# Kernel tuning notes

Hardware: AMD Instinct MI355X
Metric: run time of the kernel (lower is better)

Reference implementation:

```python
import jax, jax.numpy as jnp
import numpy as np

N_NODES = 50000
N_EDGES = 800000
D = 64
N_LAYERS = 3  # layer_dims = [64, 64, 64, 64]


def setup_inputs() -> dict:
    key = jax.random.key(0)
    ks = jax.random.split(key, 5)
    x = jax.random.normal(ks[0], (N_NODES, D), dtype=jnp.float32)
    edge_index = jax.random.randint(ks[1], (2, N_EDGES), 0, N_NODES, dtype=jnp.int64)
    scale = 1.0 / np.sqrt(D)
    # Per-layer restriction (message) maps, self-loop maps, and biases.
    W_msg = jax.random.normal(ks[2], (N_LAYERS, D, D), dtype=jnp.float32) * scale
    W_self = jax.random.normal(ks[3], (N_LAYERS, D, D), dtype=jnp.float32) * scale
    b = jax.random.normal(ks[4], (N_LAYERS, D), dtype=jnp.float32) * 0.01
    return {"x": x, "edge_index": edge_index, "W_msg": W_msg, "W_self": W_self, "b": b}


def reference(x, edge_index, W_msg, W_self, b):
    """Stacked sheaf conv layers: per-edge gather -> linear restriction ->
    scatter-sum aggregation to destination nodes + self-loop linear + bias,
    with ReLU between layers (none after the final layer)."""
    n = x.shape[0]
    src, dst = edge_index[0], edge_index[1]
    n_layers = W_msg.shape[0]
    for i in range(n_layers):
        msg = x[src] @ W_msg[i]                                   # [E, d] gather + restriction
        agg = jax.ops.segment_sum(msg, dst, num_segments=n)       # [N, d] scatter-add
        x = x @ W_self[i] + agg + b[i]                            # self-loop + aggregate + bias
        if i < n_layers - 1:
            x = jax.nn.relu(x)
    return x
```

## Files before the change

kernel.cpp:

```cpp
#include <hip/hip_runtime.h>

#define D 64

__device__ __forceinline__ unsigned short f2bf(float f) {
    unsigned u = __float_as_uint(f);
    unsigned r = (u + 0x7FFFu + ((u >> 16) & 1u)) >> 16;
    return (unsigned short)r;
}
__device__ __forceinline__ float bf2f(unsigned short h) {
    return __uint_as_float((unsigned)h << 16);
}

typedef __attribute__((ext_vector_type(8))) short bf16x8;
typedef __attribute__((ext_vector_type(4))) float f32x4;

__global__ void prep_kernel(const float* __restrict__ x, unsigned short* __restrict__ xb,
                            int total, int* __restrict__ deg, int N,
                            const float* __restrict__ Wself,
                            const float* __restrict__ Wmsg,
                            unsigned short* __restrict__ Bt, int n_layers) {
    int i = blockIdx.x * blockDim.x + threadIdx.x;
    if (i < N) deg[i] = 0;
    int wtotal = n_layers * D * 2 * D;
    if (i < wtotal) {
        int k = i & 127;
        int n = (i >> 7) & 63;
        int l = i >> 13;
        float w = (k < D) ? Wself[(size_t)l * D * D + k * D + n]
                          : Wmsg [(size_t)l * D * D + (k - D) * D + n];
        unsigned short hi = f2bf(w);
        unsigned short lo = f2bf(w - bf2f(hi));
        size_t base = (size_t)l * 2 * D * 2 * D;
        Bt[base + (size_t)n * 128 + k] = hi;
        Bt[base + 8192 + (size_t)n * 128 + k] = lo;
    }
    int base = i * 4;
    if (base + 4 <= total) {
        float4 v = *reinterpret_cast<const float4*>(x + base);
        ushort4 o;
        o.x = f2bf(v.x); o.y = f2bf(v.y); o.z = f2bf(v.z); o.w = f2bf(v.w);
        *reinterpret_cast<ushort4*>(xb + base) = o;
    } else if (base < total) {
        for (int k = base; k < total; ++k) xb[k] = f2bf(x[k]);
    }
}

__global__ void hist_rank_kernel(const int* __restrict__ dst, int* __restrict__ deg,
                                 int* __restrict__ rank, int E) {
    int i = blockIdx.x * blockDim.x + threadIdx.x;
    int base = i * 8;
    if (base + 8 <= E) {
        int4 d0 = *reinterpret_cast<const int4*>(dst + base);
        int4 d1 = *reinterpret_cast<const int4*>(dst + base + 4);
        int4 r0, r1;
        r0.x = atomicAdd(&deg[d0.x], 1);
        r0.y = atomicAdd(&deg[d0.y], 1);
        r0.z = atomicAdd(&deg[d0.z], 1);
        r0.w = atomicAdd(&deg[d0.w], 1);
        r1.x = atomicAdd(&deg[d1.x], 1);
        r1.y = atomicAdd(&deg[d1.y], 1);
        r1.z = atomicAdd(&deg[d1.z], 1);
        r1.w = atomicAdd(&deg[d1.w], 1);
        *reinterpret_cast<int4*>(rank + base) = r0;
        *reinterpret_cast<int4*>(rank + base + 4) = r1;
    } else {
        for (int e = base; e < E; ++e) rank[e] = atomicAdd(&deg[dst[e]], 1);
    }
}

__global__ void scan_k1(const int* __restrict__ deg, int* __restrict__ bsum, int n) {
    __shared__ int sh[256];
    int t = threadIdx.x;
    int g = blockIdx.x * 256 + t;
    int v = (g < n) ? deg[g] : 0;
    sh[t] = v;
    __syncthreads();
    for (int off = 1; off < 256; off <<= 1) {
        int u = (t >= off) ? sh[t - off] : 0;
        __syncthreads();
        sh[t] += u;
        __syncthreads();
    }
    if (t == 255) bsum[blockIdx.x] = sh[255];
}

__global__ void scan_k2(const int* __restrict__ bsum, int* __restrict__ boff, int nb) {
    __shared__ int sh[1024];
    int t = threadIdx.x;
    int v = (t < nb) ? bsum[t] : 0;
    sh[t] = v;
    __syncthreads();
    for (int off = 1; off < 1024; off <<= 1) {
        int u = (t >= off) ? sh[t - off] : 0;
        __syncthreads();
        sh[t] += u;
        __syncthreads();
    }
    if (t < nb) boff[t] = sh[t] - v;
}

__global__ void scan_k3(const int* __restrict__ deg, const int* __restrict__ boff,
                        int* __restrict__ row_ptr, int n) {
    __shared__ int sh[256];
    int t = threadIdx.x;
    int g = blockIdx.x * 256 + t;
    int v = (g < n) ? deg[g] : 0;
    sh[t] = v;
    __syncthreads();
    for (int off = 1; off < 256; off <<= 1) {
        int u = (t >= off) ? sh[t - off] : 0;
        __syncthreads();
        sh[t] += u;
        __syncthreads();
    }
    if (g < n) {
        int excl = sh[t] - v + boff[blockIdx.x];
        row_ptr[g] = excl;
        if (g == n - 1) row_ptr[n] = excl + v;
    }
}

__global__ void perm_rank_kernel(const int* __restrict__ src, const int* __restrict__ dst,
                                 const int* __restrict__ rank, const int* __restrict__ row_ptr,
                                 int* __restrict__ sorted_src, int E) {
    int i = blockIdx.x * blockDim.x + threadIdx.x;
    int base = i * 8;
    if (base + 8 <= E) {
        int4 d0 = *reinterpret_cast<const int4*>(dst + base);
        int4 d1 = *reinterpret_cast<const int4*>(dst + base + 4);
        int4 s0 = *reinterpret_cast<const int4*>(src + base);
        int4 s1 = *reinterpret_cast<const int4*>(src + base + 4);
        int4 r0 = *reinterpret_cast<const int4*>(rank + base);
        int4 r1 = *reinterpret_cast<const int4*>(rank + base + 4);
        int p0 = row_ptr[d0.x] + r0.x;
        int p1 = row_ptr[d0.y] + r0.y;
        int p2 = row_ptr[d0.z] + r0.z;
        int p3 = row_ptr[d0.w] + r0.w;
        int p4 = row_ptr[d1.x] + r1.x;
        int p5 = row_ptr[d1.y] + r1.y;
        int p6 = row_ptr[d1.z] + r1.z;
        int p7 = row_ptr[d1.w] + r1.w;
        __builtin_nontemporal_store(s0.x, &sorted_src[p0]);
        __builtin_nontemporal_store(s0.y, &sorted_src[p1]);
        __builtin_nontemporal_store(s0.z, &sorted_src[p2]);
        __builtin_nontemporal_store(s0.w, &sorted_src[p3]);
        __builtin_nontemporal_store(s1.x, &sorted_src[p4]);
        __builtin_nontemporal_store(s1.y, &sorted_src[p5]);
        __builtin_nontemporal_store(s1.z, &sorted_src[p6]);
        __builtin_nontemporal_store(s1.w, &sorted_src[p7]);
    } else {
        for (int e = base; e < E; ++e)
            sorted_src[row_ptr[dst[e]] + rank[e]] = src[e];
    }
}

__global__ void __launch_bounds__(256)
gather_bf16(const unsigned short* __restrict__ xb,
            const int* __restrict__ row_ptr,
            const int* __restrict__ sorted_src,
            unsigned short* __restrict__ aggb, int n_nodes, int E) {
    int lane = threadIdx.x & 63;
    int n = blockIdx.x * (blockDim.x >> 6) + (threadIdx.x >> 6);
    if (n >= n_nodes) return;
    int g = lane >> 4;
    int j = lane & 15;

    int beg = row_ptr[n];
    int end = row_ptr[n + 1];

    float ax0=0.f, ay0=0.f, az0=0.f, aw0=0.f;
    float ax1=0.f, ay1=0.f, az1=0.f, aw1=0.f;
    float ax2=0.f, ay2=0.f, az2=0.f, aw2=0.f;
    float ax3=0.f, ay3=0.f, az3=0.f, aw3=0.f;

    int e = beg + g;
    for (; e + 12 < end; e += 16) {
        int s0 = sorted_src[e];
        int s1 = sorted_src[e + 4];
        int s2 = sorted_src[e + 8];
        int s3 = sorted_src[e + 12];
        uint2 u0 = *reinterpret_cast<const uint2*>(xb + (((size_t)(unsigned)s0) << 6) + (j << 2));
        uint2 u1 = *reinterpret_cast<const uint2*>(xb + (((size_t)(unsigned)s1) << 6) + (j << 2));
        uint2 u2 = *reinterpret_cast<const uint2*>(xb + (((size_t)(unsigned)s2) << 6) + (j << 2));
        uint2 u3 = *reinterpret_cast<const uint2*>(xb + (((size_t)(unsigned)s3) << 6) + (j << 2));
        ax0 += __uint_as_float(u0.x << 16); ay0 += __uint_as_float(u0.x & 0xFFFF0000u);
        az0 += __uint_as_float(u0.y << 16); aw0 += __uint_as_float(u0.y & 0xFFFF0000u);
        ax1 += __uint_as_float(u1.x << 16); ay1 += __uint_as_float(u1.x & 0xFFFF0000u);
        az1 += __uint_as_float(u1.y << 16); aw1 += __uint_as_float(u1.y & 0xFFFF0000u);
        ax2 += __uint_as_float(u2.x << 16); ay2 += __uint_as_float(u2.x & 0xFFFF0000u);
        az2 += __uint_as_float(u2.y << 16); aw2 += __uint_as_float(u2.y & 0xFFFF0000u);
        ax3 += __uint_as_float(u3.x << 16); ay3 += __uint_as_float(u3.x & 0xFFFF0000u);
        az3 += __uint_as_float(u3.y << 16); aw3 += __uint_as_float(u3.y & 0xFFFF0000u);
    }
    {
        int e1 = e + 4, e2 = e + 8;
        bool q0 = e  < end;
        bool q1 = e1 < end;
        bool q2 = e2 < end;
        int c0 = min(e,  E - 1);
        int c1 = min(e1, E - 1);
        int c2 = min(e2, E - 1);
        int s0 = sorted_src[c0];
        int s1 = sorted_src[c1];
        int s2 = sorted_src[c2];
        uint2 u0 = *reinterpret_cast<const uint2*>(xb + (((size_t)(unsigned)s0) << 6) + (j << 2));
        uint2 u1 = *reinterpret_cast<const uint2*>(xb + (((size_t)(unsigned)s1) << 6) + (j << 2));
        uint2 u2 = *reinterpret_cast<const uint2*>(xb + (((size_t)(unsigned)s2) << 6) + (j << 2));
        if (q0) {
            ax0 += __uint_as_float(u0.x << 16); ay0 += __uint_as_float(u0.x & 0xFFFF0000u);
            az0 += __uint_as_float(u0.y << 16); aw0 += __uint_as_float(u0.y & 0xFFFF0000u);
        }
        if (q1) {
            ax1 += __uint_as_float(u1.x << 16); ay1 += __uint_as_float(u1.x & 0xFFFF0000u);
            az1 += __uint_as_float(u1.y << 16); aw1 += __uint_as_float(u1.y & 0xFFFF0000u);
        }
        if (q2) {
            ax2 += __uint_as_float(u2.x << 16); ay2 += __uint_as_float(u2.x & 0xFFFF0000u);
            az2 += __uint_as_float(u2.y << 16); aw2 += __uint_as_float(u2.y & 0xFFFF0000u);
        }
    }
    float ax = (ax0 + ax1) + (ax2 + ax3);
    float ay = (ay0 + ay1) + (ay2 + ay3);
    float az = (az0 + az1) + (az2 + az3);
    float aw = (aw0 + aw1) + (aw2 + aw3);
    ax += __shfl_xor(ax, 16); ay += __shfl_xor(ay, 16);
    az += __shfl_xor(az, 16); aw += __shfl_xor(aw, 16);
    ax += __shfl_xor(ax, 32); ay += __shfl_xor(ay, 32);
    az += __shfl_xor(az, 32); aw += __shfl_xor(aw, 32);

    if (g == 0) {
        uint2 o;
        o.x = (unsigned)f2bf(ax) | ((unsigned)f2bf(ay) << 16);
        o.y = (unsigned)f2bf(az) | ((unsigned)f2bf(aw) << 16);
        *reinterpret_cast<uint2*>(aggb + (((size_t)(unsigned)n) << 6) + (j << 2)) = o;
    }
}

__global__ void __launch_bounds__(256)
dense_mfma(const unsigned short* __restrict__ xb,
           const unsigned short* __restrict__ aggb,
           const unsigned short* __restrict__ Bt,
           const float* __restrict__ bias,
           float* __restrict__ out_f32,
           unsigned short* __restrict__ out_bf16,
           int n_nodes, int n_tiles, int last) {
    int lane = threadIdx.x & 63;
    int wave = threadIdx.x >> 6;
    int tile = blockIdx.x * (blockDim.x >> 6) + wave;
    if (tile >= n_tiles) return;

    int ln15 = lane & 15;
    int lhi  = lane >> 4;

    bf16x8 Bf[2][4][4];
    {
        const unsigned short* bp = Bt + (size_t)ln15 * 128 + lhi * 8;
#pragma unroll
        for (int p = 0; p < 2; ++p)
#pragma unroll
            for (int nf = 0; nf < 4; ++nf)
#pragma unroll
                for (int kc = 0; kc < 4; ++kc)
                    Bf[p][kc][nf] = *reinterpret_cast<const bf16x8*>(
                        bp + ((size_t)p * 64 + nf * 16) * 128 + kc * 32);
    }
    float bb[4];
#pragma unroll
    for (int nf = 0; nf < 4; ++nf) bb[nf] = bias[nf * 16 + ln15];

    int node0 = tile << 4;
    int arow = node0 + ln15;
    int acl = min(arow, n_nodes - 1);
    const unsigned short* xr = xb   + ((size_t)(unsigned)acl << 6) + lhi * 8;
    const unsigned short* ar = aggb + ((size_t)(unsigned)acl << 6) + lhi * 8;

    bf16x8 A[4];
    A[0] = *reinterpret_cast<const bf16x8*>(xr);
    A[1] = *reinterpret_cast<const bf16x8*>(xr + 32);
    A[2] = *reinterpret_cast<const bf16x8*>(ar);
    A[3] = *reinterpret_cast<const bf16x8*>(ar + 32);

#pragma unroll
    for (int nf = 0; nf < 4; ++nf) {
        f32x4 c = {0.f, 0.f, 0.f, 0.f};
#pragma unroll
        for (int kc = 0; kc < 4; ++kc) {
            c = __builtin_amdgcn_mfma_f32_16x16x32_bf16(A[kc], Bf[0][kc][nf], c, 0, 0, 0);
            c = __builtin_amdgcn_mfma_f32_16x16x32_bf16(A[kc], Bf[1][kc][nf], c, 0, 0, 0);
        }
        if (last) {
#pragma unroll
            for (int r = 0; r < 4; ++r) {
                int node = node0 + lhi * 4 + r;
                if (node < n_nodes)
                    out_f32[((size_t)(unsigned)node << 6) + nf * 16 + ln15] = c[r] + bb[nf];
            }
        } else {
#pragma unroll
            for (int r = 0; r < 4; ++r) {
                int node = node0 + lhi * 4 + r;
                if (node < n_nodes)
                    out_bf16[((size_t)(unsigned)node << 6) + nf * 16 + ln15] =
                        f2bf(fmaxf(c[r] + bb[nf], 0.f));
            }
        }
    }
}

__global__ void scatter_kernel(const float* __restrict__ x,
                               const int* __restrict__ src,
                               const int* __restrict__ dst,
                               float* __restrict__ agg, int n_edges) {
    int e = blockIdx.x * (blockDim.x >> 6) + (threadIdx.x >> 6);
    int lane = threadIdx.x & 63;
    if (e >= n_edges) return;
    float v = x[(size_t)src[e] * D + lane];
    unsafeAtomicAdd(&agg[(size_t)dst[e] * D + lane], v);
}

__global__ void dense_kernel(const float* __restrict__ xin,
                             const float* __restrict__ agg,
                             const float* __restrict__ Wself,
                             const float* __restrict__ Wmsg,
                             const float* __restrict__ bias,
                             float* __restrict__ xout,
                             int n_nodes, int do_relu) {
    __shared__ float Ws[D * D];
    __shared__ float Wm[D * D];
    for (int i = threadIdx.x; i < D * D; i += blockDim.x) {
        Ws[i] = Wself[i];
        Wm[i] = Wmsg[i];
    }
    __syncthreads();
    int lane = threadIdx.x & 63;
    int wave = threadIdx.x >> 6;
    int wpb = blockDim.x >> 6;
    float bj = bias[lane];
    for (int n = blockIdx.x * wpb + wave; n < n_nodes; n += gridDim.x * wpb) {
        float xv = xin[(size_t)n * D + lane];
        float av = agg[(size_t)n * D + lane];
        float acc = bj;
#pragma unroll
        for (int k = 0; k < D; ++k) {
            acc += __shfl(xv, k, 64) * Ws[k * D + lane]
                 + __shfl(av, k, 64) * Wm[k * D + lane];
        }
        if (do_relu) acc = fmaxf(acc, 0.f);
        xout[(size_t)n * D + lane] = acc;
    }
}

extern "C" void kernel_launch(void* const* d_in, const int* in_sizes, int n_in,
                              void* d_out, int out_size, void* d_ws, size_t ws_size,
                              hipStream_t stream) {
    const float* x0    = (const float*)d_in[0];
    const int*   ei    = (const int*)d_in[1];
    const float* Wmsg  = (const float*)d_in[2];
    const float* Wself = (const float*)d_in[3];
    const float* bias  = (const float*)d_in[4];
    float* out = (float*)d_out;

    const int N = in_sizes[0] / D;
    const int E = in_sizes[1] / 2;
    const int n_layers = in_sizes[4] / D;

    const int* src = ei;
    const int* dst = ei + E;
    const size_t NB = (size_t)N * D * sizeof(float);

    const int NBB = (N + 255) / 256;
    const size_t BtB = (size_t)n_layers * 2 * D * 2 * D * 2;
    const size_t need = (size_t)N * D * 2
                      + (size_t)N * D * 2
                      + BtB
                      + (size_t)E * 4
                      + (size_t)E * 4
                      + (size_t)(N + 1) * 4
                      + (size_t)N * 4
                      + (size_t)NBB * 4 * 2 + 256;

    if (ws_size >= need && NBB <= 1024) {
        char* p = (char*)d_ws;
        unsigned short* Xb   = (unsigned short*)p;  p += (size_t)N * D * 2;
        unsigned short* Aggb = (unsigned short*)p;  p += (size_t)N * D * 2;
        unsigned short* Bt   = (unsigned short*)p;  p += BtB;
        int* sorted_src      = (int*)p;             p += (size_t)E * 4;
        int* rank            = (int*)p;             p += (size_t)E * 4;
        int* row_ptr         = (int*)p;             p += (size_t)(N + 1) * 4;
        int* deg             = (int*)p;             p += (size_t)N * 4;
        int* bsum            = (int*)p;             p += (size_t)NBB * 4;
        int* boff            = (int*)p;

        {
            int total = N * D;
            int nthr = (total + 3) / 4;
            prep_kernel<<<(nthr + 255) / 256, 256, 0, stream>>>(
                x0, Xb, total, deg, N, Wself, Wmsg, Bt, n_layers);

            int threads = 256;
            int nthr8 = (E + 7) / 8;
            int blocks = (nthr8 + threads - 1) / threads;
            hist_rank_kernel<<<blocks, threads, 0, stream>>>(dst, deg, rank, E);
            scan_k1<<<NBB, 256, 0, stream>>>(deg, bsum, N);
            scan_k2<<<1, 1024, 0, stream>>>(bsum, boff, NBB);
            scan_k3<<<NBB, 256, 0, stream>>>(deg, boff, row_ptr, N);
            perm_rank_kernel<<<blocks, threads, 0, stream>>>(src, dst, rank, row_ptr,
                                                             sorted_src, E);
        }

        const int gather_blocks = (N + 3) / 4;
        const int dtiles = (N + 15) >> 4;
        const int dblocks = (dtiles + 3) >> 2;

        for (int layer = 0; layer < n_layers; ++layer) {
            gather_bf16<<<gather_blocks, 256, 0, stream>>>(Xb, row_ptr, sorted_src,
                                                           Aggb, N, E);
            dense_mfma<<<dblocks, 256, 0, stream>>>(
                Xb, Aggb,
                Bt + (size_t)layer * 2 * D * 2 * D,
                bias + (size_t)layer * D,
                out, Xb, N, dtiles, (layer == n_layers - 1) ? 1 : 0);
        }
    } else {
        float* agg = (float*)d_ws;
        const int EPB = 256 / 64;
        const int scatter_blocks = (E + EPB - 1) / EPB;
        for (int layer = 0; layer < n_layers; ++layer) {
            hipMemsetAsync(agg, 0, NB, stream);
            const float* xin = (layer == 0) ? x0 : out;
            scatter_kernel<<<scatter_blocks, 256, 0, stream>>>(xin, src, dst, agg, E);
            dense_kernel<<<1024, 256, 0, stream>>>(
                xin, agg,
                Wself + (size_t)layer * D * D,
                Wmsg  + (size_t)layer * D * D,
                bias  + (size_t)layer * D,
                out, N, (layer < n_layers - 1) ? 1 : 0);
        }
    }
}
```

Before: 275.7 us.

## Fuse neighbor gather and MFMA dense update into one per-layer kernel

Replaces the separate gather kernel and dense MFMA kernel with a single fused kernel per layer. Each block handles 16 nodes: its four waves split each node's edges by stride, accumulate bf16 rows in fp32 registers, reduce through shared memory, and each wave then computes 16 output columns with MFMA. The bf16 aggregate no longer round-trips through global memory and one launch per layer is removed; input and output feature buffers are now ping-ponged because the fused kernel reads neighbors while writing. In exchange, edge loops are bounded by the maximum degree in each 16-node group, which can leave lanes idle under degree imbalance, and the block reduction needs a barrier.

```diff
diff --git a/kernel.cpp b/kernel.cpp
--- a/kernel.cpp
+++ b/kernel.cpp
@@ -154,155 +154,150 @@
     }
 }
 
+__device__ __forceinline__ void acc16(float* ac, uint4 u0, uint4 u1) {
+    ac[0]  += __uint_as_float(u0.x << 16);
+    ac[1]  += __uint_as_float(u0.x & 0xFFFF0000u);
+    ac[2]  += __uint_as_float(u0.y << 16);
+    ac[3]  += __uint_as_float(u0.y & 0xFFFF0000u);
+    ac[4]  += __uint_as_float(u0.z << 16);
+    ac[5]  += __uint_as_float(u0.z & 0xFFFF0000u);
+    ac[6]  += __uint_as_float(u0.w << 16);
+    ac[7]  += __uint_as_float(u0.w & 0xFFFF0000u);
+    ac[8]  += __uint_as_float(u1.x << 16);
+    ac[9]  += __uint_as_float(u1.x & 0xFFFF0000u);
+    ac[10] += __uint_as_float(u1.y << 16);
+    ac[11] += __uint_as_float(u1.y & 0xFFFF0000u);
+    ac[12] += __uint_as_float(u1.z << 16);
+    ac[13] += __uint_as_float(u1.z & 0xFFFF0000u);
+    ac[14] += __uint_as_float(u1.w << 16);
+    ac[15] += __uint_as_float(u1.w & 0xFFFF0000u);
+}
+
 __global__ void __launch_bounds__(256)
-gather_bf16(const unsigned short* __restrict__ xb,
+fused_layer(const unsigned short* __restrict__ xb,
             const int* __restrict__ row_ptr,
             const int* __restrict__ sorted_src,
-            unsigned short* __restrict__ aggb, int n_nodes, int E) {
+            const unsigned short* __restrict__ Bt,
+            const float* __restrict__ bias,
+            float* __restrict__ out_f32,
+            unsigned short* __restrict__ out_bf16,
+            int n_nodes, int E, int last) {
+    __shared__ float red[4][16][68];
+
     int lane = threadIdx.x & 63;
-    int n = blockIdx.x * (blockDim.x >> 6) + (threadIdx.x >> 6);
-    if (n >= n_nodes) return;
-    int g = lane >> 4;
-    int j = lane & 15;
-
-    int beg = row_ptr[n];
-    int end = row_ptr[n + 1];
-
-    float ax0=0.f, ay0=0.f, az0=0.f, aw0=0.f;
-    float ax1=0.f, ay1=0.f, az1=0.f, aw1=0.f;
-    float ax2=0.f, ay2=0.f, az2=0.f, aw2=0.f;
-    float ax3=0.f, ay3=0.f, az3=0.f, aw3=0.f;
-
-    int e = beg + g;
-    for (; e + 12 < end; e += 16) {
-        int s0 = sorted_src[e];
-        int s1 = sorted_src[e + 4];
-        int s2 = sorted_src[e + 8];
-        int s3 = sorted_src[e + 12];
-        uint2 u0 = *reinterpret_cast<const uint2*>(xb + (((size_t)(unsigned)s0) << 6) + (j << 2));
-        uint2 u1 = *reinterpret_cast<const uint2*>(xb + (((size_t)(unsigned)s1) << 6) + (j << 2));
-        uint2 u2 = *reinterpret_cast<const uint2*>(xb + (((size_t)(unsigned)s2) << 6) + (j << 2));
-        uint2 u3 = *reinterpret_cast<const uint2*>(xb + (((size_t)(unsigned)s3) << 6) + (j << 2));
-        ax0 += __uint_as_float(u0.x << 16); ay0 += __uint_as_float(u0.x & 0xFFFF0000u);
-        az0 += __uint_as_float(u0.y << 16); aw0 += __uint_as_float(u0.y & 0xFFFF0000u);
-        ax1 += __uint_as_float(u1.x << 16); ay1 += __uint_as_float(u1.x & 0xFFFF0000u);
-        az1 += __uint_as_float(u1.y << 16); aw1 += __uint_as_float(u1.y & 0xFFFF0000u);
-        ax2 += __uint_as_float(u2.x << 16); ay2 += __uint_as_float(u2.x & 0xFFFF0000u);
-        az2 += __uint_as_float(u2.y << 16); aw2 += __uint_as_float(u2.y & 0xFFFF0000u);
-        ax3 += __uint_as_float(u3.x << 16); ay3 += __uint_as_float(u3.x & 0xFFFF0000u);
-        az3 += __uint_as_float(u3.y << 16); aw3 += __uint_as_float(u3.y & 0xFFFF0000u);
-    }
-    {
-        int e1 = e + 4, e2 = e + 8;
-        bool q0 = e  < end;
-        bool q1 = e1 < end;
-        bool q2 = e2 < end;
-        int c0 = min(e,  E - 1);
-        int c1 = min(e1, E - 1);
-        int c2 = min(e2, E - 1);
-        int s0 = sorted_src[c0];
-        int s1 = sorted_src[c1];
-        int s2 = sorted_src[c2];
-        uint2 u0 = *reinterpret_cast<const uint2*>(xb + (((size_t)(unsigned)s0) << 6) + (j << 2));
-        uint2 u1 = *reinterpret_cast<const uint2*>(xb + (((size_t)(unsigned)s1) << 6) + (j << 2));
-        uint2 u2 = *reinterpret_cast<const uint2*>(xb + (((size_t)(unsigned)s2) << 6) + (j << 2));
-        if (q0) {
-            ax0 += __uint_as_float(u0.x << 16); ay0 += __uint_as_float(u0.x & 0xFFFF0000u);
-            az0 += __uint_as_float(u0.y << 16); aw0 += __uint_as_float(u0.y & 0xFFFF0000u);
-        }
-        if (q1) {
-            ax1 += __uint_as_float(u1.x << 16); ay1 += __uint_as_float(u1.x & 0xFFFF0000u);
-            az1 += __uint_as_float(u1.y << 16); aw1 += __uint_as_float(u1.y & 0xFFFF0000u);
-        }
-        if (q2) {
-            ax2 += __uint_as_float(u2.x << 16); ay2 += __uint_as_float(u2.x & 0xFFFF0000u);
-            az2 += __uint_as_float(u2.y << 16); aw2 += __uint_as_float(u2.y & 0xFFFF0000u);
-        }
-    }
-    float ax = (ax0 + ax1) + (ax2 + ax3);
-    float ay = (ay0 + ay1) + (ay2 + ay3);
-    float az = (az0 + az1) + (az2 + az3);
-    float aw = (aw0 + aw1) + (aw2 + aw3);
-    ax += __shfl_xor(ax, 16); ay += __shfl_xor(ay, 16);
-    az += __shfl_xor(az, 16); aw += __shfl_xor(aw, 16);
-    ax += __shfl_xor(ax, 32); ay += __shfl_xor(ay, 32);
-    az += __shfl_xor(az, 32); aw += __shfl_xor(aw, 32);
-
-    if (g == 0) {
-        uint2 o;
-        o.x = (unsigned)f2bf(ax) | ((unsigned)f2bf(ay) << 16);
-        o.y = (unsigned)f2bf(az) | ((unsigned)f2bf(aw) << 16);
-        *reinterpret_cast<uint2*>(aggb + (((size_t)(unsigned)n) << 6) + (j << 2)) = o;
-    }
-}
-
-__global__ void __launch_bounds__(256)
-dense_mfma(const unsigned short* __restrict__ xb,
-           const unsigned short* __restrict__ aggb,
-           const unsigned short* __restrict__ Bt,
-           const float* __restrict__ bias,
-           float* __restrict__ out_f32,
-           unsigned short* __restrict__ out_bf16,
-           int n_nodes, int n_tiles, int last) {
-    int lane = threadIdx.x & 63;
-    int wave = threadIdx.x >> 6;
-    int tile = blockIdx.x * (blockDim.x >> 6) + wave;
-    if (tile >= n_tiles) return;
-
+    int w    = threadIdx.x >> 6;
     int ln15 = lane & 15;
     int lhi  = lane >> 4;
 
-    bf16x8 Bf[2][4][4];
+    int node0 = blockIdx.x << 4;
+    int node  = node0 + ln15;
+    int ncl   = min(node, n_nodes - 1);
+    int beg = row_ptr[ncl];
+    int end = row_ptr[ncl + 1];
+    if (node >= n_nodes) end = beg;
+    int deg = end - beg;
+
+    int md = deg;
+    md = max(md, __shfl_xor(md, 1));
+    md = max(md, __shfl_xor(md, 2));
+    md = max(md, __shfl_xor(md, 4));
+    md = max(md, __shfl_xor(md, 8));
+
+    float ac[16];
+#pragma unroll
+    for (int t = 0; t < 16; ++t) ac[t] = 0.f;
+
+    const int Em1 = E - 1;
+    int p = w;
+    for (; p + 4 < md; p += 8) {
+        int cA = min(beg + p,     Em1);
+        int cB = min(beg + p + 4, Em1);
+        int sA = sorted_src[cA];
+        int sB = sorted_src[cB];
+        const unsigned short* rA = xb + (((size_t)(unsigned)sA) << 6) + (lhi << 3);
+        const unsigned short* rB = xb + (((size_t)(unsigned)sB) << 6) + (lhi << 3);
+        uint4 a0 = *reinterpret_cast<const uint4*>(rA);
+        uint4 a1 = *reinterpret_cast<const uint4*>(rA + 32);
+        uint4 b0 = *reinterpret_cast<const uint4*>(rB);
+        uint4 b1 = *reinterpret_cast<const uint4*>(rB + 32);
+        if (p < deg)     acc16(ac, a0, a1);
+        if (p + 4 < deg) acc16(ac, b0, b1);
+    }
+    for (; p < md; p += 4) {
+        int cA = min(beg + p, Em1);
+        int sA = sorted_src[cA];
+        const unsigned short* rA = xb + (((size_t)(unsigned)sA) << 6) + (lhi << 3);
+        uint4 a0 = *reinterpret_cast<const uint4*>(rA);
+        uint4 a1 = *reinterpret_cast<const uint4*>(rA + 32);
+        if (p < deg) acc16(ac, a0, a1);
+    }
+
+    int f0 = lhi << 3;
+    *reinterpret_cast<float4*>(&red[w][ln15][f0])      = make_float4(ac[0], ac[1], ac[2], ac[3]);
+    *reinterpret_cast<float4*>(&red[w][ln15][f0 + 4])  = make_float4(ac[4], ac[5], ac[6], ac[7]);
+    *reinterpret_cast<float4*>(&red[w][ln15][32 + f0]) = make_float4(ac[8], ac[9], ac[10], ac[11]);
+    *reinterpret_cast<float4*>(&red[w][ln15][36 + f0]) = make_float4(ac[12], ac[13], ac[14], ac[15]);
+
+    bf16x8 Bf[2][4];
     {
-        const unsigned short* bp = Bt + (size_t)ln15 * 128 + lhi * 8;
-#pragma unroll
-        for (int p = 0; p < 2; ++p)
-#pragma unroll
-            for (int nf = 0; nf < 4; ++nf)
-#pragma unroll
-                for (int kc = 0; kc < 4; ++kc)
-                    Bf[p][kc][nf] = *reinterpret_cast<const bf16x8*>(
-                        bp + ((size_t)p * 64 + nf * 16) * 128 + kc * 32);
-    }
-    float bb[4];
-#pragma unroll
-    for (int nf = 0; nf < 4; ++nf) bb[nf] = bias[nf * 16 + ln15];
-
-    int node0 = tile << 4;
-    int arow = node0 + ln15;
-    int acl = min(arow, n_nodes - 1);
-    const unsigned short* xr = xb   + ((size_t)(unsigned)acl << 6) + lhi * 8;
-    const unsigned short* ar = aggb + ((size_t)(unsigned)acl << 6) + lhi * 8;
-
-    bf16x8 A[4];
-    A[0] = *reinterpret_cast<const bf16x8*>(xr);
-    A[1] = *reinterpret_cast<const bf16x8*>(xr + 32);
-    A[2] = *reinterpret_cast<const bf16x8*>(ar);
-    A[3] = *reinterpret_cast<const bf16x8*>(ar + 32);
-
-#pragma unroll
-    for (int nf = 0; nf < 4; ++nf) {
-        f32x4 c = {0.f, 0.f, 0.f, 0.f};
-#pragma unroll
-        for (int kc = 0; kc < 4; ++kc) {
-            c = __builtin_amdgcn_mfma_f32_16x16x32_bf16(A[kc], Bf[0][kc][nf], c, 0, 0, 0);
-            c = __builtin_amdgcn_mfma_f32_16x16x32_bf16(A[kc], Bf[1][kc][nf], c, 0, 0, 0);
-        }
-        if (last) {
-#pragma unroll
-            for (int r = 0; r < 4; ++r) {
-                int node = node0 + lhi * 4 + r;
-                if (node < n_nodes)
-                    out_f32[((size_t)(unsigned)node << 6) + nf * 16 + ln15] = c[r] + bb[nf];
-            }
-        } else {
-#pragma unroll
-            for (int r = 0; r < 4; ++r) {
-                int node = node0 + lhi * 4 + r;
-                if (node < n_nodes)
-                    out_bf16[((size_t)(unsigned)node << 6) + nf * 16 + ln15] =
-                        f2bf(fmaxf(c[r] + bb[nf], 0.f));
-            }
+        const unsigned short* bp = Bt + ((size_t)(w * 16 + ln15)) * 128 + (lhi << 3);
+#pragma unroll
+        for (int pp = 0; pp < 2; ++pp)
+#pragma unroll
+            for (int kc = 0; kc < 4; ++kc)
+                Bf[pp][kc] = *reinterpret_cast<const bf16x8*>(bp + pp * 8192 + kc * 32);
+    }
+    const unsigned short* xr = xb + (((size_t)(unsigned)ncl) << 6) + (lhi << 3);
+    bf16x8 A0 = *reinterpret_cast<const bf16x8*>(xr);
+    bf16x8 A1 = *reinterpret_cast<const bf16x8*>(xr + 32);
+    float bb = bias[w * 16 + ln15];
+
+    __syncthreads();
+
+    float s[16];
+#pragma unroll
+    for (int t = 0; t < 16; ++t) s[t] = 0.f;
+#pragma unroll
+    for (int ww = 0; ww < 4; ++ww) {
+        float4 r0 = *reinterpret_cast<const float4*>(&red[ww][ln15][f0]);
+        float4 r1 = *reinterpret_cast<const float4*>(&red[ww][ln15][f0 + 4]);
+        float4 r2 = *reinterpret_cast<const float4*>(&red[ww][ln15][32 + f0]);
+        float4 r3 = *reinterpret_cast<const float4*>(&red[ww][ln15][36 + f0]);
+        s[0]  += r0.x; s[1]  += r0.y; s[2]  += r0.z; s[3]  += r0.w;
+        s[4]  += r1.x; s[5]  += r1.y; s[6]  += r1.z; s[7]  += r1.w;
+        s[8]  += r2.x; s[9]  += r2.y; s[10] += r2.z; s[11] += r2.w;
+        s[12] += r3.x; s[13] += r3.y; s[14] += r3.z; s[15] += r3.w;
+    }
+    bf16x8 A2, A3;
+#pragma unroll
+    for (int t = 0; t < 8; ++t) A2[t] = (short)f2bf(s[t]);
+#pragma unroll
+    for (int t = 0; t < 8; ++t) A3[t] = (short)f2bf(s[8 + t]);
+
+    f32x4 c = {0.f, 0.f, 0.f, 0.f};
+    c = __builtin_amdgcn_mfma_f32_16x16x32_bf16(A0, Bf[0][0], c, 0, 0, 0);
+    c = __builtin_amdgcn_mfma_f32_16x16x32_bf16(A0, Bf[1][0], c, 0, 0, 0);
+    c = __builtin_amdgcn_mfma_f32_16x16x32_bf16(A1, Bf[0][1], c, 0, 0, 0);
+    c = __builtin_amdgcn_mfma_f32_16x16x32_bf16(A1, Bf[1][1], c, 0, 0, 0);
+    c = __builtin_amdgcn_mfma_f32_16x16x32_bf16(A2, Bf[0][2], c, 0, 0, 0);
+    c = __builtin_amdgcn_mfma_f32_16x16x32_bf16(A2, Bf[1][2], c, 0, 0, 0);
+    c = __builtin_amdgcn_mfma_f32_16x16x32_bf16(A3, Bf[0][3], c, 0, 0, 0);
+    c = __builtin_amdgcn_mfma_f32_16x16x32_bf16(A3, Bf[1][3], c, 0, 0, 0);
+
+    int colo = w * 16 + ln15;
+    if (last) {
+#pragma unroll
+        for (int r = 0; r < 4; ++r) {
+            int nr = node0 + lhi * 4 + r;
+            if (nr < n_nodes)
+                out_f32[((size_t)(unsigned)nr << 6) + colo] = c[r] + bb;
+        }
+    } else {
+#pragma unroll
+        for (int r = 0; r < 4; ++r) {
+            int nr = node0 + lhi * 4 + r;
+            if (nr < n_nodes)
+                out_bf16[((size_t)(unsigned)nr << 6) + colo] = f2bf(fmaxf(c[r] + bb, 0.f));
         }
     }
 }
@@ -382,7 +377,7 @@
     if (ws_size >= need && NBB <= 1024) {
         char* p = (char*)d_ws;
         unsigned short* Xb   = (unsigned short*)p;  p += (size_t)N * D * 2;
-        unsigned short* Aggb = (unsigned short*)p;  p += (size_t)N * D * 2;
+        unsigned short* Xb2  = (unsigned short*)p;  p += (size_t)N * D * 2;
         unsigned short* Bt   = (unsigned short*)p;  p += BtB;
         int* sorted_src      = (int*)p;             p += (size_t)E * 4;
         int* rank            = (int*)p;             p += (size_t)E * 4;
@@ -408,18 +403,19 @@
                                                              sorted_src, E);
         }
 
-        const int gather_blocks = (N + 3) / 4;
         const int dtiles = (N + 15) >> 4;
-        const int dblocks = (dtiles + 3) >> 2;
+        const unsigned short* in_b = Xb;
+        unsigned short* out_b = Xb2;
 
         for (int layer = 0; layer < n_layers; ++layer) {
-            gather_bf16<<<gather_blocks, 256, 0, stream>>>(Xb, row_ptr, sorted_src,
-                                                           Aggb, N, E);
-            dense_mfma<<<dblocks, 256, 0, stream>>>(
-                Xb, Aggb,
+            fused_layer<<<dtiles, 256, 0, stream>>>(
+                in_b, row_ptr, sorted_src,
                 Bt + (size_t)layer * 2 * D * 2 * D,
                 bias + (size_t)layer * D,
-                out, Xb, N, dtiles, (layer == n_layers - 1) ? 1 : 0);
+                out, out_b, N, E, (layer == n_layers - 1) ? 1 : 0);
+            const unsigned short* t = in_b;
+            in_b = out_b;
+            out_b = (unsigned short*)t;
         }
     } else {
         float* agg = (float*)d_ws;
```

New measurement: 255.1 us. 1.08x faster.
